# Kernel tuning notes

Hardware: AMD Instinct MI355X
Metric: run time of the kernel (lower is better)

Reference implementation:

```python
import jax, jax.numpy as jnp
import numpy as np

B, A, V, H, F, ND, NC, NE, NL = 4096, 768, 2048, 512, 1024, 16, 2, 8, 3


def setup_inputs() -> dict:
    key = jax.random.key(0)
    ks = jax.random.split(key, 16)

    def g(k, shape, fan_in):
        return jax.random.normal(k, shape, jnp.float32) * (1.0 / np.sqrt(fan_in))

    return {
        "audio": jax.random.normal(ks[0], (B, A), jnp.float32),
        "video": jax.random.normal(ks[1], (B, V), jnp.float32),
        "disease_idx": jax.random.randint(ks[2], (B,), 0, ND),
        "Wa": g(ks[3], (A, H), A), "ba": jnp.zeros((H,), jnp.float32),
        "Wv": g(ks[4], (V, H), V), "bv": jnp.zeros((H,), jnp.float32),
        "Pa": g(ks[5], (H, F), H), "Cva": g(ks[6], (H, F), H),
        "Pv": g(ks[7], (H, F), H), "Cav": g(ks[8], (H, F), H),
        "Wproj": g(ks[9], (2 * F, F), 2 * F), "bproj": jnp.zeros((F,), jnp.float32),
        "Wf": g(ks[10], (NL, F, F), F), "bf": jnp.zeros((NL, F), jnp.float32),
        "Wc1": g(ks[11], (ND, F, 256), F), "bc1": jnp.zeros((ND, 256), jnp.float32),
        "Wc2": g(ks[12], (ND, 256, NC), 256), "bc2": jnp.zeros((ND, NC), jnp.float32),
        "We1": g(ks[13], (H, 128), H), "be1": jnp.zeros((128,), jnp.float32),
        "We2": g(ks[14], (128, NE), 128), "be2": jnp.zeros((NE,), jnp.float32),
    }


def reference(audio, video, disease_idx, Wa, ba, Wv, bv, Pa, Cva, Pv, Cav,
              Wproj, bproj, Wf, bf, Wc1, bc1, Wc2, bc2, We1, be1, We2, be2):
    # Audio / video feature encoders (stand-ins for AudioModel / VideoModel)
    af = jax.nn.relu(audio @ Wa + ba)            # (B, H)
    vf = jax.nn.relu(video @ Wv + bv)            # (B, H)

    # Cross-modal mixing block: each stream attends to (mixes in) the other
    attended_audio = af @ Pa + vf @ Cva          # (B, F)
    attended_video = vf @ Pv + af @ Cav          # (B, F)

    # Concat fusion; 2F != F so the on-the-fly fusion projection is applied
    fused = jnp.concatenate([attended_audio, attended_video], axis=1)  # (B, 2F)
    fused = fused @ Wproj + bproj                # (B, F)

    # Fusion MLP: NL x (Linear -> ReLU), trailing Dropout stripped (inference)
    for i in range(NL):
        fused = jax.nn.relu(fused @ Wf[i] + bf[i])

    # Disease-indexed per-sample head dispatch.
    # Reference computes all heads densely then gathers by disease_idx —
    # identical math to the per-sample Python loop in the torch code.
    h_all = jax.nn.relu(jnp.einsum("bf,nfh->bnh", fused, Wc1) + bc1)   # (B, ND, 256)
    l_all = jnp.einsum("bnh,nhc->bnc", h_all, Wc2) + bc2               # (B, ND, NC)
    logits = jnp.take_along_axis(l_all, disease_idx[:, None, None], axis=1)[:, 0, :]  # (B, NC)

    # Auxiliary emotion head on video features
    emotion_logits = jax.nn.relu(vf @ We1 + be1) @ We2 + be2            # (B, NE)

    return logits, af, vf, fused, emotion_logits
```

## Files before the change

kernel.cpp:

```cpp
#include <hip/hip_runtime.h>
#include <hip/hip_bf16.h>
#include <stdint.h>


typedef __attribute__((ext_vector_type(8))) short bf16x8;
typedef __attribute__((ext_vector_type(4))) float f32x4;

__device__ inline short f2b(float f) {
  union { float f; uint32_t u; } a; a.f = f;
  uint32_t r = a.u + 0x7fffu + ((a.u >> 16) & 1u);
  return (short)(r >> 16);
}
__device__ inline float b2f(short s) {
  union { uint32_t u; float f; } a; a.u = ((uint32_t)(uint16_t)s) << 16;
  return a.f;
}
__device__ inline void gload_lds16(const void* g, void* l) {
  __builtin_amdgcn_global_load_lds(
      (const __attribute__((address_space(1))) uint32_t*)g,
      (__attribute__((address_space(3))) uint32_t*)l, 16, 0, 0);
}
template<int N> __device__ __forceinline__ void waitv() {
  asm volatile("s_waitcnt vmcnt(%0)" :: "n"(N) : "memory");
}

__device__ __forceinline__
void transpose_tile(const float* __restrict__ in, short* __restrict__ out,
                    int N, int ldout, int n0, int k0, short* scratch) {
  short (*t)[66] = (short(*)[66])scratch;
  const int tid = threadIdx.x;
#pragma unroll
  for (int p = 0; p < 4; ++p) {
    const int item = p * 256 + tid;
    const int row = item >> 4, c4 = (item & 15) << 2;
    float4 v = *(const float4*)(in + (long)(k0 + row) * N + n0 + c4);
    short4 o; o.x = f2b(v.x); o.y = f2b(v.y); o.z = f2b(v.z); o.w = f2b(v.w);
    *(short4*)&t[row][c4] = o;
  }
  __syncthreads();
#pragma unroll
  for (int p = 0; p < 4; ++p) {
    const int item = p * 256 + tid;
    const int kg4 = item & 15, n = item >> 4;
    short4 o;
    o.x = t[4 * kg4 + 0][n]; o.y = t[4 * kg4 + 1][n];
    o.z = t[4 * kg4 + 2][n]; o.w = t[4 * kg4 + 3][n];
    *(short4*)(out + (long)(n0 + n) * ldout + k0 + 4 * kg4) = o;
  }
}

__global__ __launch_bounds__(256)
void prep_k(const float* __restrict__ Wa, const float* __restrict__ Wv,
            const float* __restrict__ Wproj,
            const float* __restrict__ Pa, const float* __restrict__ Cva,
            const float* __restrict__ Cav, const float* __restrict__ Pv,
            const float* __restrict__ audio, const float* __restrict__ video,
            short* __restrict__ WaT, short* __restrict__ WvT,
            short* __restrict__ WprojT, short* __restrict__ Watt,
            short* __restrict__ a_bf, short* __restrict__ v_bf) {
  __shared__ short t[64 * 66];
  int b = blockIdx.x;
  const int tid = threadIdx.x;

  if (b >= 1376) {
    const float* in; short* out;
    if (b < 2144) { b -= 1376; in = audio; out = a_bf; }
    else          { b -= 2144; in = video; out = v_bf; }
    const long base_ = (long)b * 4096;
#pragma unroll
    for (int p = 0; p < 4; ++p) {
      const long i = base_ + ((p * 256 + tid) << 2);
      float4 v = *(const float4*)(in + i);
      short4 o; o.x = f2b(v.x); o.y = f2b(v.y); o.z = f2b(v.z); o.w = f2b(v.w);
      *(short4*)(out + i) = o;
    }
    return;
  }
  if (b >= 864) {
    b -= 864;
    const int q = b >> 7, r4 = (b & 127) << 2;
    const float* src; int rowoff, coloff;
    if (q == 0)      { src = Pa;  rowoff = 0;   coloff = 0; }
    else if (q == 1) { src = Cav; rowoff = 0;   coloff = 1024; }
    else if (q == 2) { src = Cva; rowoff = 512; coloff = 0; }
    else             { src = Pv;  rowoff = 512; coloff = 1024; }
#pragma unroll
    for (int p = 0; p < 4; ++p) {
      const int item = p * 256 + tid;
      const int h = r4 + (item >> 8), j = (item & 255) << 2;
      float4 v = *(const float4*)(src + (long)h * 1024 + j);
      short4 o; o.x = f2b(v.x); o.y = f2b(v.y); o.z = f2b(v.z); o.w = f2b(v.w);
      *(short4*)(Watt + (long)(rowoff + h) * 2048 + coloff + j) = o;
    }
    return;
  }
  const float* in; short* out; int N, ldout, nnb;
  if (b < 96)       { in = Wa;    out = WaT;    N = 512;  ldout = 768;  nnb = 8; }
  else if (b < 352) { b -= 96;  in = Wv;    out = WvT;    N = 512;  ldout = 2048; nnb = 8; }
  else              { b -= 352; in = Wproj; out = WprojT; N = 1024; ldout = 2048; nnb = 16; }
  transpose_tile(in, out, N, ldout, (b % nnb) << 6, (b / nnb) << 6, t);
}

template<int BM, int BN, bool RELU, bool HASF32>
__device__ __forceinline__
void gemm_body(const short* __restrict__ A, const short* __restrict__ BT,
               const float* __restrict__ bias,
               short* __restrict__ Cb, int ldcb,
               float* __restrict__ Cf, int ldcf,
               int K, int lda, int ldbt, int m0, int n0,
               short* lds) {
  constexpr int MR = BM / 32, NR = BN / 32;
  constexpr int S = MR + NR;
  constexpr int BUF = (BM + BN) * 64;
  const int tid = threadIdx.x;
  const int w = tid >> 6, l = tid & 63;
  const int wr = w >> 1, wc = w & 1;
  const int lr = l & 15, lk = (l >> 4) << 3;

  f32x4 acc[MR][NR];
#pragma unroll
  for (int m = 0; m < MR; ++m)
#pragma unroll
    for (int n = 0; n < NR; ++n) acc[m][n] = (f32x4)0.f;

  const int r_ = tid >> 3;
  const int kc_ = (((tid & 7) ^ (r_ & 7)) << 3);
  const short* Arow = A + (long)(m0 + r_) * lda + kc_;
  const short* Brow = BT + (long)(n0 + r_) * ldbt + kc_;
  const int nk = K >> 6;

  auto stage = [&](int t, int buf) {
    const int kt = t << 6;
    char* sA = (char*)(lds + buf * BUF);
    char* sB = sA + BM * 128;
#pragma unroll
    for (int i = 0; i < MR; ++i)
      gload_lds16(Arow + (long)i * 32 * lda + kt, sA + i * 4096 + w * 1024);
#pragma unroll
    for (int i = 0; i < NR; ++i)
      gload_lds16(Brow + (long)i * 32 * ldbt + kt, sB + i * 4096 + w * 1024);
  };

  stage(0, 0);
  int cur = 0;
  for (int t = 0; t < nk; ++t) {
    __builtin_amdgcn_s_barrier();
    __builtin_amdgcn_sched_barrier(0);
    if (t + 1 < nk) {
      stage(t + 1, cur ^ 1);
      waitv<S>();
    } else {
      waitv<0>();
    }
    __builtin_amdgcn_s_barrier();
    __builtin_amdgcn_sched_barrier(0);
    const short* sA = lds + cur * BUF;
    const short* sB = sA + BM * 64;
#pragma unroll
    for (int kk = 0; kk < 64; kk += 32) {
      const int cb = (kk + lk) >> 3;
      bf16x8 a[MR], b[NR];
#pragma unroll
      for (int m = 0; m < MR; ++m) {
        const int ra = wr * (BM / 2) + m * 16 + lr;
        a[m] = *(const bf16x8*)&sA[ra * 64 + ((cb ^ (ra & 7)) << 3)];
      }
#pragma unroll
      for (int n = 0; n < NR; ++n) {
        const int rb = wc * (BN / 2) + n * 16 + lr;
        b[n] = *(const bf16x8*)&sB[rb * 64 + ((cb ^ (rb & 7)) << 3)];
      }
#pragma unroll
      for (int m = 0; m < MR; ++m)
#pragma unroll
        for (int n = 0; n < NR; ++n)
          acc[m][n] = __builtin_amdgcn_mfma_f32_16x16x32_bf16(a[m], b[n], acc[m][n], 0, 0, 0);
    }
    __builtin_amdgcn_sched_barrier(0);
    cur ^= 1;
  }

  const int lrow = (l >> 4) << 2;
#pragma unroll
  for (int n = 0; n < NR; ++n) {
    const int col = n0 + wc * (BN / 2) + n * 16 + lr;
    const float bz = bias ? bias[col] : 0.f;
#pragma unroll
    for (int m = 0; m < MR; ++m) {
      const int rowb = m0 + wr * (BM / 2) + m * 16 + lrow;
#pragma unroll
      for (int i = 0; i < 4; ++i) {
        float v = acc[m][n][i] + bz;
        if (RELU) v = fmaxf(v, 0.f);
        Cb[(long)(rowb + i) * ldcb + col] = f2b(v);
        if (HASF32) Cf[(long)(rowb + i) * ldcf + col] = v;
      }
    }
  }
}

template<int BM, int BN, bool RELU, bool HASF32>
__global__ __launch_bounds__(256, 3)
void gemm_bt(const short* __restrict__ A, const short* __restrict__ BT,
             const float* __restrict__ bias,
             short* __restrict__ Cb, int ldcb,
             float* __restrict__ Cf, int ldcf,
             int K, int lda, int ldbt) {
  __shared__ short lds[2 * (BM + BN) * 64];
  gemm_body<BM, BN, RELU, HASF32>(A, BT, bias, Cb, ldcb, Cf, ldcf,
                                  K, lda, ldbt, blockIdx.x * BM, blockIdx.y * BN,
                                  lds);
}

__global__ __launch_bounds__(256, 3)
void enc_w2t_k(const short* __restrict__ a_bf, const short* __restrict__ v_bf,
               const short* __restrict__ WaT, const short* __restrict__ WvT,
               const float* __restrict__ ba, const float* __restrict__ bv,
               short* __restrict__ afvf, float* __restrict__ out_af,
               float* __restrict__ out_vf,
               const short* __restrict__ WprojT, const short* __restrict__ Watt_rm,
               short* __restrict__ W2T,
               const float* __restrict__ Wf, const float* __restrict__ Wc1,
               const float* __restrict__ We1,
               short* __restrict__ WfT, short* __restrict__ Wc1T,
               short* __restrict__ We1T,
               const int* __restrict__ didx, int* __restrict__ perm,
               int* __restrict__ bstart, int* __restrict__ bmap) {
  __shared__ short lds[2 * (128 + 64) * 64];
  int b = blockIdx.x;
  const int tid = threadIdx.x;
  if (b < 512) {
    const int x = b & 31, y = b >> 5;
    const bool isA = y < 8;
    gemm_body<128, 64, true, true>(
        isA ? a_bf : v_bf, isA ? WaT : WvT, isA ? ba : bv,
        afvf + (isA ? 0 : 512), 1024, isA ? out_af : out_vf, 512,
        isA ? 768 : 2048, isA ? 768 : 2048, isA ? 768 : 2048,
        x << 7, (y & 7) << 6, lds);
  } else if (b < 1024) {
    b -= 512;
    gemm_body<64, 32, false, false>(
        WprojT, Watt_rm, nullptr, W2T, 1024, nullptr, 0,
        2048, 2048, 2048, (b & 15) << 6, (b >> 4) << 5, lds);
  } else if (b < 2832) {
    b -= 1024;
    const float* in; short* out; int N, ldout, nnb;
    if (b < 768)       { int z = b >> 8; b &= 255;
                         in = Wf + (long)z * 1048576; out = WfT + (long)z * 1048576;
                         N = 1024; ldout = 1024; nnb = 16; }
    else if (b < 1792) { b -= 768; int z = b >> 6; b &= 63;
                         in = Wc1 + (long)z * 262144; out = Wc1T + (long)z * 262144;
                         N = 256; ldout = 1024; nnb = 4; }
    else               { b -= 1792; in = We1; out = We1T; N = 128; ldout = 512; nnb = 2; }
    transpose_tile(in, out, N, ldout, (b % nnb) << 6, (b / nnb) << 6, lds);
  } else {
    int* cnt = (int*)lds; int* base = cnt + 16; int* curp = base + 17;
    if (tid < 16) cnt[tid] = 0;
    __syncthreads();
    for (int r = tid; r < 4096; r += 256) atomicAdd(&cnt[didx[r]], 1);
    __syncthreads();
    if (tid == 0) {
      int s = 0;
      for (int d = 0; d < 16; ++d) { base[d] = s; s += cnt[d]; }
      base[16] = s;
      int nb = 0;
      for (int d = 0; d < 16; ++d) {
        int nblk = (cnt[d] + 63) >> 6;
        for (int i = 0; i < nblk; ++i) bmap[nb++] = (d << 8) | i;
      }
      bstart[17] = nb;
    }
    __syncthreads();
    if (tid < 16) curp[tid] = base[tid];
    if (tid < 17) bstart[tid] = base[tid];
    __syncthreads();
    for (int r = tid; r < 4096; r += 256) {
      int p = atomicAdd(&curp[didx[r]], 1);
      perm[p] = r;
    }
  }
}

__global__ __launch_bounds__(256, 3)
void g34emo_k(const short* __restrict__ afvf, const short* __restrict__ W2T,
              const float* __restrict__ bproj, short* __restrict__ fusedA,
              const short* __restrict__ We1T, const float* __restrict__ be1,
              short* __restrict__ e1_bf) {
  __shared__ short lds[2 * (128 + 64) * 64];
  int b = blockIdx.x;
  if (b < 512) {
    gemm_body<128, 64, false, false>(
        afvf, W2T, bproj, fusedA, 1024, nullptr, 0,
        1024, 1024, 1024, (b & 31) << 7, (b >> 5) << 6, lds);
  } else {
    b -= 512;
    gemm_body<64, 32, true, false>(
        afvf + 512, We1T, be1, e1_bf, 128, nullptr, 0,
        512, 1024, 512, (b & 63) << 6, (b >> 6) << 5, lds);
  }
}

__global__ __launch_bounds__(256, 3)
void head_gemm(const short* __restrict__ fused, const short* __restrict__ Wc1T,
               const float* __restrict__ bc1, const int* __restrict__ perm,
               const int* __restrict__ bstart, const int* __restrict__ bmap,
               short* __restrict__ h) {
  const int nb = bstart[17];
  if ((int)blockIdx.x >= nb) return;
  const int me = bmap[blockIdx.x];
  const int d = me >> 8, rt = me & 0xff;
  const int b0 = bstart[d], cnt = bstart[d + 1] - b0;
  const int t0 = rt << 6;
  const int c0 = blockIdx.y << 6;
  __shared__ short lds[2 * 128 * 64];
  const int tid = threadIdx.x, w = tid >> 6, l = tid & 63;
  const int wr = w >> 1, wc = w & 1;
  const int lr = l & 15, lk = (l >> 4) << 3;
  const short* BT = Wc1T + (long)d * (256 * 1024) + (long)c0 * 1024;

  f32x4 acc[2][2];
#pragma unroll
  for (int m = 0; m < 2; ++m)
#pragma unroll
    for (int n = 0; n < 2; ++n) acc[m][n] = (f32x4)0.f;

  const int r_ = tid >> 3;
  const int kc_ = (((tid & 7) ^ (r_ & 7)) << 3);
  int gr0 = (t0 + r_      < cnt) ? perm[b0 + t0 + r_]      : perm[b0];
  int gr1 = (t0 + r_ + 32 < cnt) ? perm[b0 + t0 + r_ + 32] : perm[b0];
  const short* A0 = fused + (long)gr0 * 1024 + kc_;
  const short* A1 = fused + (long)gr1 * 1024 + kc_;
  const short* Brow = BT + (long)r_ * 1024 + kc_;

  auto stage = [&](int t, int buf) {
    const int kt = t << 6;
    char* sA = (char*)lds + buf * 16384;
    char* sB = sA + 8192;
    gload_lds16(A0 + kt, sA + w * 1024);
    gload_lds16(A1 + kt, sA + 4096 + w * 1024);
    gload_lds16(Brow + kt, sB + w * 1024);
    gload_lds16(Brow + 32 * 1024 + kt, sB + 4096 + w * 1024);
  };

  stage(0, 0);
  int cur = 0;
  for (int t = 0; t < 16; ++t) {
    __builtin_amdgcn_s_barrier();
    __builtin_amdgcn_sched_barrier(0);
    if (t + 1 < 16) {
      stage(t + 1, cur ^ 1);
      waitv<4>();
    } else {
      waitv<0>();
    }
    __builtin_amdgcn_s_barrier();
    __builtin_amdgcn_sched_barrier(0);
    const short* sA = lds + cur * 8192;
    const short* sB = sA + 4096;
#pragma unroll
    for (int kk = 0; kk < 64; kk += 32) {
      const int cb = (kk + lk) >> 3;
      bf16x8 a[2], b[2];
#pragma unroll
      for (int m = 0; m < 2; ++m) {
        const int ra = wr * 32 + m * 16 + lr;
        a[m] = *(const bf16x8*)&sA[ra * 64 + ((cb ^ (ra & 7)) << 3)];
      }
#pragma unroll
      for (int n = 0; n < 2; ++n) {
        const int rb = wc * 32 + n * 16 + lr;
        b[n] = *(const bf16x8*)&sB[rb * 64 + ((cb ^ (rb & 7)) << 3)];
      }
#pragma unroll
      for (int m = 0; m < 2; ++m)
#pragma unroll
        for (int n = 0; n < 2; ++n)
          acc[m][n] = __builtin_amdgcn_mfma_f32_16x16x32_bf16(a[m], b[n], acc[m][n], 0, 0, 0);
    }
    __builtin_amdgcn_sched_barrier(0);
    cur ^= 1;
  }

#pragma unroll
  for (int m = 0; m < 2; ++m)
#pragma unroll
    for (int i2 = 0; i2 < 4; ++i2) {
      const int lrow = wr * 32 + m * 16 + ((l >> 4) << 2) + i2;
      if (t0 + lrow >= cnt) continue;
      const int gr = perm[b0 + t0 + lrow];
#pragma unroll
      for (int n = 0; n < 2; ++n) {
        const int col = c0 + wc * 32 + n * 16 + lr;
        float v = acc[m][n][i2] + bc1[d * 256 + col];
        v = fmaxf(v, 0.f);
        h[(long)gr * 256 + col] = f2b(v);
      }
    }
}

__global__ __launch_bounds__(256)
void tail_k(const short* __restrict__ h, const float* __restrict__ Wc2,
            const float* __restrict__ bc2, const int* __restrict__ didx,
            const short* __restrict__ e1, const float* __restrict__ We2,
            const float* __restrict__ be2,
            float* __restrict__ out_logits, float* __restrict__ out_emo) {
  const int w = threadIdx.x >> 6, l = threadIdx.x & 63;
  if (blockIdx.x < 1024) {
    const int r = ((int)blockIdx.x << 2) + w;
    const int d = didx[r];
    const short4 hv4 = *(const short4*)(h + (long)r * 256 + (l << 2));
    const float* wr_ = Wc2 + d * 512 + (l << 3);
    const float4 w01 = *(const float4*)wr_;
    const float4 w23 = *(const float4*)(wr_ + 4);
    const float h0 = b2f(hv4.x), h1 = b2f(hv4.y), h2 = b2f(hv4.z), h3 = b2f(hv4.w);
    float a0 = h0 * w01.x + h1 * w01.z + h2 * w23.x + h3 * w23.z;
    float a1 = h0 * w01.y + h1 * w01.w + h2 * w23.y + h3 * w23.w;
#pragma unroll
    for (int off = 32; off > 0; off >>= 1) {
      a0 += __shfl_down(a0, off);
      a1 += __shfl_down(a1, off);
    }
    if (l == 0) {
      out_logits[r * 2 + 0] = a0 + bc2[d * 2 + 0];
      out_logits[r * 2 + 1] = a1 + bc2[d * 2 + 1];
    }
  } else {
    const int r = (((int)blockIdx.x - 1024) << 2) + w;
    const float h0 = b2f(e1[(long)r * 128 + 2 * l]);
    const float h1 = b2f(e1[(long)r * 128 + 2 * l + 1]);
    const float* w0 = We2 + (2 * l) * 8;
    float a[8];
#pragma unroll
    for (int c = 0; c < 8; ++c) a[c] = h0 * w0[c] + h1 * w0[8 + c];
#pragma unroll
    for (int c = 0; c < 8; ++c)
#pragma unroll
      for (int off = 32; off > 0; off >>= 1) a[c] += __shfl_down(a[c], off);
    if (l == 0) {
#pragma unroll
      for (int c = 0; c < 8; ++c) out_emo[r * 8 + c] = a[c] + be2[c];
    }
  }
}

extern "C" void kernel_launch(void* const* d_in, const int* in_sizes, int n_in,
                              void* d_out, int out_size, void* d_ws, size_t ws_size,
                              hipStream_t stream) {
  const float* audio = (const float*)d_in[0];
  const float* video = (const float*)d_in[1];
  const int*   didx  = (const int*)d_in[2];
  const float* Wa    = (const float*)d_in[3];
  const float* ba    = (const float*)d_in[4];
  const float* Wv    = (const float*)d_in[5];
  const float* bv    = (const float*)d_in[6];
  const float* Pa    = (const float*)d_in[7];
  const float* Cva   = (const float*)d_in[8];
  const float* Pv    = (const float*)d_in[9];
  const float* Cav   = (const float*)d_in[10];
  const float* Wproj = (const float*)d_in[11];
  const float* bproj = (const float*)d_in[12];
  const float* Wf    = (const float*)d_in[13];
  const float* bfv   = (const float*)d_in[14];
  const float* Wc1   = (const float*)d_in[15];
  const float* bc1   = (const float*)d_in[16];
  const float* Wc2   = (const float*)d_in[17];
  const float* bc2   = (const float*)d_in[18];
  const float* We1   = (const float*)d_in[19];
  const float* be1   = (const float*)d_in[20];
  const float* We2   = (const float*)d_in[21];
  const float* be2   = (const float*)d_in[22];

  char* ws = (char*)d_ws;
  short* W2T     = (short*)(ws + 0);
  short* WaT     = (short*)(ws + 2097152);
  short* WvT     = (short*)(ws + 2883584);
  short* Watt_rm = (short*)(ws + 4980736);
  short* WprojT  = (short*)(ws + 9175040);
  short* WfT     = (short*)(ws + 13369344);
  short* Wc1T    = (short*)(ws + 19660800);
  short* We1T    = (short*)(ws + 28049408);
  short* afvf    = (short*)(ws + 28180480);
  short* fusedA  = (short*)(ws + 36569088);
  short* fusedB  = (short*)(ws + 44957696);
  short* h_bf    = (short*)(ws + 53346304);
  short* e1_bf   = (short*)(ws + 55443456);
  int*   perm    = (int*)(ws + 56492032);
  int*   bstart  = (int*)(ws + 56508416);
  int*   bmap    = (int*)(ws + 56508544);
  short* a_bf    = (short*)(ws + 56512512);
  short* v_bf    = (short*)(ws + 62803968);

  float* out        = (float*)d_out;
  float* out_logits = out;
  float* out_af     = out + 8192;
  float* out_vf     = out + 2105344;
  float* out_fused  = out + 4202496;
  float* out_emo    = out + 8396800;

  prep_k<<<dim3(4192), dim3(256), 0, stream>>>(
      Wa, Wv, Wproj, Pa, Cva, Cav, Pv, audio, video,
      WaT, WvT, WprojT, Watt_rm, a_bf, v_bf);

  enc_w2t_k<<<dim3(2833), dim3(256), 0, stream>>>(
      a_bf, v_bf, WaT, WvT, ba, bv, afvf, out_af, out_vf,
      WprojT, Watt_rm, W2T,
      Wf, Wc1, We1, WfT, Wc1T, We1T,
      didx, perm, bstart, bmap);

  g34emo_k<<<dim3(768), dim3(256), 0, stream>>>(
      afvf, W2T, bproj, fusedA, We1T, be1, e1_bf);

  gemm_bt<128, 64, true, false><<<dim3(32, 16), dim3(256), 0, stream>>>(
      fusedA, WfT, bfv, fusedB, 1024, nullptr, 0, 1024, 1024, 1024);
  gemm_bt<128, 64, true, false><<<dim3(32, 16), dim3(256), 0, stream>>>(
      fusedB, WfT + 1048576, bfv + 1024, fusedA, 1024, nullptr, 0, 1024, 1024, 1024);
  gemm_bt<128, 64, true, true><<<dim3(32, 16), dim3(256), 0, stream>>>(
      fusedA, WfT + 2097152, bfv + 2048, fusedB, 1024, out_fused, 1024, 1024, 1024, 1024);

  head_gemm<<<dim3(80, 4), dim3(256), 0, stream>>>(fusedB, Wc1T, bc1, perm, bstart, bmap, h_bf);
  tail_k<<<dim3(2048), dim3(256), 0, stream>>>(
      h_bf, Wc2, bc2, didx, e1_bf, We2, be2, out_logits, out_emo);
}
```

Measured before the change: 130.2 us.

## Fuse classifier second layer into head GEMM with atomics, swizzle GEMM tiles

The second classifier layer (256→2) now runs in the head GEMM epilogue. Each block reduces partial dot products across lanes and atomically adds them into logits, which are pre-initialised with the bias by an extra block in the fused-projection kernel. This removes the h intermediate buffer and the separate tail kernel, and the emotion-head tail moves into extra blocks of the head kernel. GEMM block indices are swizzled for better L2 locality, and encoder blocks are reordered so the video GEMM (largest K) starts first. Float atomics make logit summation order nondeterministic.

```diff
diff --git a/kernel.cpp b/kernel.cpp
--- a/kernel.cpp
+++ b/kernel.cpp
@@ -207,9 +207,11 @@
              float* __restrict__ Cf, int ldcf,
              int K, int lda, int ldbt) {
   __shared__ short lds[2 * (BM + BN) * 64];
+  const int lin = blockIdx.y * 32 + blockIdx.x;
+  const int swz = (lin & 7) * 64 + (lin >> 3);
   gemm_body<BM, BN, RELU, HASF32>(A, BT, bias, Cb, ldcb, Cf, ldcf,
-                                  K, lda, ldbt, blockIdx.x * BM, blockIdx.y * BN,
-                                  lds);
+                                  K, lda, ldbt,
+                                  (swz & 31) << 7, (swz >> 5) << 6, lds);
 }
 
 __global__ __launch_bounds__(256, 3)
@@ -230,18 +232,19 @@
   int b = blockIdx.x;
   const int tid = threadIdx.x;
   if (b < 512) {
-    const int x = b & 31, y = b >> 5;
-    const bool isA = y < 8;
+    gemm_body<64, 32, false, false>(
+        WprojT, Watt_rm, nullptr, W2T, 1024, nullptr, 0,
+        2048, 2048, 2048, (b & 15) << 6, (b >> 4) << 5, lds);
+  } else if (b < 1024) {
+    b -= 512;
+    const bool isA = b >= 256;
+    const int vb = isA ? b - 256 : b;
+    const int x = vb & 31, y8 = vb >> 5;
     gemm_body<128, 64, true, true>(
         isA ? a_bf : v_bf, isA ? WaT : WvT, isA ? ba : bv,
         afvf + (isA ? 0 : 512), 1024, isA ? out_af : out_vf, 512,
         isA ? 768 : 2048, isA ? 768 : 2048, isA ? 768 : 2048,
-        x << 7, (y & 7) << 6, lds);
-  } else if (b < 1024) {
-    b -= 512;
-    gemm_body<64, 32, false, false>(
-        WprojT, Watt_rm, nullptr, W2T, 1024, nullptr, 0,
-        2048, 2048, 2048, (b & 15) << 6, (b >> 4) << 5, lds);
+        x << 7, y8 << 6, lds);
   } else if (b < 2832) {
     b -= 1024;
     const float* in; short* out; int N, ldout, nnb;
@@ -285,35 +288,66 @@
 void g34emo_k(const short* __restrict__ afvf, const short* __restrict__ W2T,
               const float* __restrict__ bproj, short* __restrict__ fusedA,
               const short* __restrict__ We1T, const float* __restrict__ be1,
-              short* __restrict__ e1_bf) {
+              short* __restrict__ e1_bf,
+              const int* __restrict__ didx, const float* __restrict__ bc2,
+              float* __restrict__ out_logits) {
   __shared__ short lds[2 * (128 + 64) * 64];
   int b = blockIdx.x;
   if (b < 512) {
+    const int swz = (b & 7) * 64 + (b >> 3);
     gemm_body<128, 64, false, false>(
         afvf, W2T, bproj, fusedA, 1024, nullptr, 0,
-        1024, 1024, 1024, (b & 31) << 7, (b >> 5) << 6, lds);
-  } else {
+        1024, 1024, 1024, (swz & 31) << 7, (swz >> 5) << 6, lds);
+  } else if (b < 768) {
     b -= 512;
     gemm_body<64, 32, true, false>(
         afvf + 512, We1T, be1, e1_bf, 128, nullptr, 0,
         512, 1024, 512, (b & 63) << 6, (b >> 6) << 5, lds);
+  } else {
+    for (int r = threadIdx.x; r < 4096; r += 256) {
+      const int d = didx[r];
+      out_logits[2 * r + 0] = bc2[2 * d + 0];
+      out_logits[2 * r + 1] = bc2[2 * d + 1];
+    }
   }
 }
 
 __global__ __launch_bounds__(256, 3)
-void head_gemm(const short* __restrict__ fused, const short* __restrict__ Wc1T,
-               const float* __restrict__ bc1, const int* __restrict__ perm,
-               const int* __restrict__ bstart, const int* __restrict__ bmap,
-               short* __restrict__ h) {
+void head_k(const short* __restrict__ fused, const short* __restrict__ Wc1T,
+            const float* __restrict__ bc1, const int* __restrict__ perm,
+            const int* __restrict__ bstart, const int* __restrict__ bmap,
+            const float* __restrict__ Wc2, float* __restrict__ out_logits,
+            const short* __restrict__ e1, const float* __restrict__ We2,
+            const float* __restrict__ be2, float* __restrict__ out_emo) {
+  const int tid = threadIdx.x;
+  const int w = tid >> 6, l = tid & 63;
+  if (blockIdx.x >= 320) {
+    const int r = (((int)blockIdx.x - 320) << 2) + w;
+    const float h0 = b2f(e1[(long)r * 128 + 2 * l]);
+    const float h1 = b2f(e1[(long)r * 128 + 2 * l + 1]);
+    const float* w0 = We2 + (2 * l) * 8;
+    float a[8];
+#pragma unroll
+    for (int c = 0; c < 8; ++c) a[c] = h0 * w0[c] + h1 * w0[8 + c];
+#pragma unroll
+    for (int c = 0; c < 8; ++c)
+#pragma unroll
+      for (int off = 32; off > 0; off >>= 1) a[c] += __shfl_down(a[c], off);
+    if (l == 0) {
+#pragma unroll
+      for (int c = 0; c < 8; ++c) out_emo[r * 8 + c] = a[c] + be2[c];
+    }
+    return;
+  }
+  const int hx = (int)blockIdx.x % 80, hy = (int)blockIdx.x / 80;
   const int nb = bstart[17];
-  if ((int)blockIdx.x >= nb) return;
-  const int me = bmap[blockIdx.x];
+  if (hx >= nb) return;
+  const int me = bmap[hx];
   const int d = me >> 8, rt = me & 0xff;
   const int b0 = bstart[d], cnt = bstart[d + 1] - b0;
   const int t0 = rt << 6;
-  const int c0 = blockIdx.y << 6;
+  const int c0 = hy << 6;
   __shared__ short lds[2 * 128 * 64];
-  const int tid = threadIdx.x, w = tid >> 6, l = tid & 63;
   const int wr = w >> 1, wc = w & 1;
   const int lr = l & 15, lk = (l >> 4) << 3;
   const short* BT = Wc1T + (long)d * (256 * 1024) + (long)c0 * 1024;
@@ -386,61 +420,26 @@
 #pragma unroll
     for (int i2 = 0; i2 < 4; ++i2) {
       const int lrow = wr * 32 + m * 16 + ((l >> 4) << 2) + i2;
-      if (t0 + lrow >= cnt) continue;
-      const int gr = perm[b0 + t0 + lrow];
+      float p0 = 0.f, p1 = 0.f;
 #pragma unroll
       for (int n = 0; n < 2; ++n) {
         const int col = c0 + wc * 32 + n * 16 + lr;
         float v = acc[m][n][i2] + bc1[d * 256 + col];
         v = fmaxf(v, 0.f);
-        h[(long)gr * 256 + col] = f2b(v);
-      }
-    }
-}
-
-__global__ __launch_bounds__(256)
-void tail_k(const short* __restrict__ h, const float* __restrict__ Wc2,
-            const float* __restrict__ bc2, const int* __restrict__ didx,
-            const short* __restrict__ e1, const float* __restrict__ We2,
-            const float* __restrict__ be2,
-            float* __restrict__ out_logits, float* __restrict__ out_emo) {
-  const int w = threadIdx.x >> 6, l = threadIdx.x & 63;
-  if (blockIdx.x < 1024) {
-    const int r = ((int)blockIdx.x << 2) + w;
-    const int d = didx[r];
-    const short4 hv4 = *(const short4*)(h + (long)r * 256 + (l << 2));
-    const float* wr_ = Wc2 + d * 512 + (l << 3);
-    const float4 w01 = *(const float4*)wr_;
-    const float4 w23 = *(const float4*)(wr_ + 4);
-    const float h0 = b2f(hv4.x), h1 = b2f(hv4.y), h2 = b2f(hv4.z), h3 = b2f(hv4.w);
-    float a0 = h0 * w01.x + h1 * w01.z + h2 * w23.x + h3 * w23.z;
-    float a1 = h0 * w01.y + h1 * w01.w + h2 * w23.y + h3 * w23.w;
-#pragma unroll
-    for (int off = 32; off > 0; off >>= 1) {
-      a0 += __shfl_down(a0, off);
-      a1 += __shfl_down(a1, off);
-    }
-    if (l == 0) {
-      out_logits[r * 2 + 0] = a0 + bc2[d * 2 + 0];
-      out_logits[r * 2 + 1] = a1 + bc2[d * 2 + 1];
-    }
-  } else {
-    const int r = (((int)blockIdx.x - 1024) << 2) + w;
-    const float h0 = b2f(e1[(long)r * 128 + 2 * l]);
-    const float h1 = b2f(e1[(long)r * 128 + 2 * l + 1]);
-    const float* w0 = We2 + (2 * l) * 8;
-    float a[8];
-#pragma unroll
-    for (int c = 0; c < 8; ++c) a[c] = h0 * w0[c] + h1 * w0[8 + c];
-#pragma unroll
-    for (int c = 0; c < 8; ++c)
-#pragma unroll
-      for (int off = 32; off > 0; off >>= 1) a[c] += __shfl_down(a[c], off);
-    if (l == 0) {
-#pragma unroll
-      for (int c = 0; c < 8; ++c) out_emo[r * 8 + c] = a[c] + be2[c];
-    }
-  }
+        p0 += v * Wc2[d * 512 + col * 2 + 0];
+        p1 += v * Wc2[d * 512 + col * 2 + 1];
+      }
+#pragma unroll
+      for (int off = 8; off >= 1; off >>= 1) {
+        p0 += __shfl_xor(p0, off);
+        p1 += __shfl_xor(p1, off);
+      }
+      if (lr == 0 && t0 + lrow < cnt) {
+        const int gr = perm[b0 + t0 + lrow];
+        atomicAdd(&out_logits[gr * 2 + 0], p0);
+        atomicAdd(&out_logits[gr * 2 + 1], p1);
+      }
+    }
 }
 
 extern "C" void kernel_launch(void* const* d_in, const int* in_sizes, int n_in,
@@ -482,7 +481,6 @@
   short* afvf    = (short*)(ws + 28180480);
   short* fusedA  = (short*)(ws + 36569088);
   short* fusedB  = (short*)(ws + 44957696);
-  short* h_bf    = (short*)(ws + 53346304);
   short* e1_bf   = (short*)(ws + 55443456);
   int*   perm    = (int*)(ws + 56492032);
   int*   bstart  = (int*)(ws + 56508416);
@@ -507,8 +505,8 @@
       Wf, Wc1, We1, WfT, Wc1T, We1T,
       didx, perm, bstart, bmap);
 
-  g34emo_k<<<dim3(768), dim3(256), 0, stream>>>(
-      afvf, W2T, bproj, fusedA, We1T, be1, e1_bf);
+  g34emo_k<<<dim3(769), dim3(256), 0, stream>>>(
+      afvf, W2T, bproj, fusedA, We1T, be1, e1_bf, didx, bc2, out_logits);
 
   gemm_bt<128, 64, true, false><<<dim3(32, 16), dim3(256), 0, stream>>>(
       fusedA, WfT, bfv, fusedB, 1024, nullptr, 0, 1024, 1024, 1024);
@@ -517,7 +515,7 @@
   gemm_bt<128, 64, true, true><<<dim3(32, 16), dim3(256), 0, stream>>>(
       fusedA, WfT + 2097152, bfv + 2048, fusedB, 1024, out_fused, 1024, 1024, 1024, 1024);
 
-  head_gemm<<<dim3(80, 4), dim3(256), 0, stream>>>(fusedB, Wc1T, bc1, perm, bstart, bmap, h_bf);
-  tail_k<<<dim3(2048), dim3(256), 0, stream>>>(
-      h_bf, Wc2, bc2, didx, e1_bf, We2, be2, out_logits, out_emo);
-}
+  head_k<<<dim3(1344), dim3(256), 0, stream>>>(
+      fusedB, Wc1T, bc1, perm, bstart, bmap, Wc2, out_logits,
+      e1_bf, We2, be2, out_emo);
+}
```

Measured after the change: 140.0 us. +7.5%, slower.
